# Performance work log

Hardware: AMD Instinct MI355X
Metric: run time of the kernel (lower is better)

The kernel has to match this reference:

```python
import jax, jax.numpy as jnp
import numpy as np

jax.config.update("jax_enable_x64", True)

# --- static config (matches init_kwargs) ---
L = 6            # voxel_level_num
F = 8            # feature_dim
T = 524288       # per-level feature table size
B = 4194304      # buffer_size (hash table size)
N = 1048576      # number of query points
LEAF = 0.25      # leaf_voxel_size
UP = 2.0         # up_scale_factor

PRIMES = jnp.array([73856093, 19349669, 83492791], dtype=jnp.int64)
# corner offsets, z varies fastest (same order as torch self.steps)
STEPS = jnp.array([[0,0,0],[0,0,1],[0,1,0],[0,1,1],
                   [1,0,0],[1,0,1],[1,1,0],[1,1,1]], dtype=jnp.float32)


def setup_inputs() -> dict:
    key = jax.random.key(0)
    k1, k2, k3, k4 = jax.random.split(key, 4)
    query_points = jax.random.uniform(k1, (N, 3), dtype=jnp.float32) * 50.0
    features = 0.01 * jax.random.normal(k2, (L, T, F), dtype=jnp.float32)
    idx = jax.random.randint(k3, (L, B), 0, T, dtype=jnp.int64)
    empty = jax.random.uniform(k4, (L, B)) < 0.2
    feature_indexs = jnp.where(empty, jnp.int64(-1), idx)
    return {"query_points": query_points, "features": features,
            "feature_indexs": feature_indexs}


def _trilinear_coeffs(d):
    # d: [N,3] fractional coords in the cell; order matches STEPS (z fastest)
    tx, ty, tz = d[:, 0], d[:, 1], d[:, 2]
    return jnp.stack([
        (1-tx)*(1-ty)*(1-tz), (1-tx)*(1-ty)*tz,
        (1-tx)*ty*(1-tz),     (1-tx)*ty*tz,
        tx*(1-ty)*(1-tz),     tx*(1-ty)*tz,
        tx*ty*(1-tz),         tx*ty*tz,
    ], axis=1)  # [N,8]


def reference(query_points, features, feature_indexs):
    out = jnp.zeros((query_points.shape[0], F), dtype=query_points.dtype)
    for i in range(L):  # small fixed level loop (structurally distinct resolutions)
        res = LEAF * (UP ** i)
        scaled = query_points / res                      # [N,3]
        base = jnp.floor(scaled)
        corners = (base[:, None, :] + STEPS[None]).astype(jnp.int64)  # [N,8,3]
        keys = jnp.mod((corners * PRIMES).sum(-1), B)    # [N,8] spatial hash
        idx = feature_indexs[i][keys]                    # [N,8] gather, -1 = empty
        valid = idx.min(axis=1) > -1                     # [N] all 8 corners allocated
        coeffs = _trilinear_coeffs(scaled - base)        # [N,8]
        feats = features[i][jnp.clip(idx, 0, T - 1)]     # [N,8,F] gather
        level = jnp.einsum('nkf,nk->nf', feats, coeffs)  # trilinear interp
        out = out + jnp.where(valid[:, None], level, jnp.zeros((), out.dtype))
    return out
```

## Files before the change

### kernel.cpp

```cpp
#include <hip/hip_runtime.h>


static constexpr int      NPTS  = 1048576;
static constexpr int      LVLS  = 6;
static constexpr int      NF    = 8;
static constexpr int      TTAB  = 524288;
static constexpr unsigned BTAB  = 4194304u;
static constexpr unsigned BMASK = BTAB - 1u;
static constexpr unsigned P0 = 73856093u, P1 = 19349669u, P2 = 83492791u;

static constexpr int NBIN = 4096;
static constexpr int SB   = 256;
static constexpr int PPB  = NPTS / SB;
static constexpr int ITER = PPB / 256;

__device__ __forceinline__ void nhv_point(
    float qx, float qy, float qz,
    const float* __restrict__ feat, const int* __restrict__ fidx, float acc[NF])
{
    float    fx[LVLS], fy[LVLS], fz[LVLS];
    unsigned h[LVLS];
#pragma unroll
    for (int i = 0; i < LVLS; ++i) {
        const float inv = 4.0f / (float)(1 << i);
        const float sx = qx * inv, sy = qy * inv, sz = qz * inv;
        const float bx = floorf(sx), by = floorf(sy), bz = floorf(sz);
        fx[i] = sx - bx; fy[i] = sy - by; fz[i] = sz - bz;
        h[i] = (unsigned)(int)bx * P0 + (unsigned)(int)by * P1 + (unsigned)(int)bz * P2;
    }

    int id[LVLS][8];
#pragma unroll
    for (int i = 0; i < LVLS; ++i) {
        const int* __restrict__ tab = fidx + (size_t)i * BTAB;
#pragma unroll
        for (int k = 0; k < 8; ++k) {
            unsigned key = h[i];
            if (k & 4) key += P0;
            if (k & 2) key += P1;
            if (k & 1) key += P2;
            id[i][k] = tab[key & BMASK];
        }
    }

#pragma unroll
    for (int f = 0; f < NF; ++f) acc[f] = 0.0f;

#pragma unroll
    for (int i = 0; i < LVLS; ++i) {
        int mn = id[i][0];
#pragma unroll
        for (int k = 1; k < 8; ++k) mn = min(mn, id[i][k]);
        if (mn > -1) {
            const float wxv[2] = {1.0f - fx[i], fx[i]};
            const float wyv[2] = {1.0f - fy[i], fy[i]};
            const float wzv[2] = {1.0f - fz[i], fz[i]};
            const float* __restrict__ fb = feat + (size_t)i * (TTAB * NF);
#pragma unroll
            for (int k = 0; k < 8; ++k) {
                const float c = wxv[(k >> 2) & 1] * wyv[(k >> 1) & 1] * wzv[k & 1];
                const float4* p = (const float4*)(fb + (size_t)id[i][k] * NF);
                const float4 lo = p[0];
                const float4 hi = p[1];
                acc[0] += c * lo.x; acc[1] += c * lo.y;
                acc[2] += c * lo.z; acc[3] += c * lo.w;
                acc[4] += c * hi.x; acc[5] += c * hi.y;
                acc[6] += c * hi.z; acc[7] += c * hi.w;
            }
        }
    }
}

__device__ __forceinline__ unsigned expand4(unsigned v) {
    return (v & 1u) | ((v & 2u) << 2) | ((v & 4u) << 4) | ((v & 8u) << 6);
}
__device__ __forceinline__ unsigned bin_of(float x, float y, float z) {
    unsigned bx = min(15u, (unsigned)(int)(x * 0.32f));
    unsigned by = min(15u, (unsigned)(int)(y * 0.32f));
    unsigned bz = min(15u, (unsigned)(int)(z * 0.32f));
    return expand4(bx) | (expand4(by) << 1) | (expand4(bz) << 2);
}

__global__ __launch_bounds__(256) void hist_k(const float* __restrict__ qp,
                                              unsigned* __restrict__ hist) {
    __shared__ unsigned lh[NBIN];
    const int b = blockIdx.x, t = threadIdx.x;
    for (int i = t; i < NBIN; i += 256) lh[i] = 0u;
    __syncthreads();
    const int base = b * PPB;
#pragma unroll
    for (int i = 0; i < ITER; ++i) {
        const int p = base + i * 256 + t;
        atomicAdd(&lh[bin_of(qp[3*p], qp[3*p+1], qp[3*p+2])], 1u);
    }
    __syncthreads();
    for (int i = t; i < NBIN; i += 256) hist[(size_t)b * NBIN + i] = lh[i];
}

__global__ __launch_bounds__(256) void colscan_k(unsigned* __restrict__ hist,
                                                 unsigned* __restrict__ binbase) {
    const int bin = blockIdx.x * 256 + threadIdx.x;
    unsigned run = 0;
    for (int b = 0; b < SB; ++b) {
        const unsigned v = hist[(size_t)b * NBIN + bin];
        hist[(size_t)b * NBIN + bin] = run;
        run += v;
    }
    binbase[bin] = run;
}

__global__ __launch_bounds__(256) void binscan_k(unsigned* __restrict__ binbase) {
    __shared__ unsigned tot[256];
    const int t = threadIdx.x;
    unsigned v[16];
    unsigned s = 0;
#pragma unroll
    for (int i = 0; i < 16; ++i) { v[i] = s; s += binbase[t * 16 + i]; }
    tot[t] = s;
    __syncthreads();
    for (int d = 1; d < 256; d <<= 1) {
        const unsigned x = (t >= d) ? tot[t - d] : 0u;
        __syncthreads();
        tot[t] += x;
        __syncthreads();
    }
    const unsigned cb = tot[t] - s;
#pragma unroll
    for (int i = 0; i < 16; ++i) binbase[t * 16 + i] = cb + v[i];
}

__global__ __launch_bounds__(256) void scatter_k(const float* __restrict__ qp,
                                                 const unsigned* __restrict__ hist,
                                                 const unsigned* __restrict__ binbase,
                                                 float4* __restrict__ sorted) {
    __shared__ unsigned cur[NBIN];
    const int b = blockIdx.x, t = threadIdx.x;
    for (int i = t; i < NBIN; i += 256)
        cur[i] = binbase[i] + hist[(size_t)b * NBIN + i];
    __syncthreads();
    const int base = b * PPB;
#pragma unroll
    for (int i = 0; i < ITER; ++i) {
        const int p = base + i * 256 + t;
        const float x = qp[3*p], y = qp[3*p+1], z = qp[3*p+2];
        const unsigned slot = atomicAdd(&cur[bin_of(x, y, z)], 1u);
        sorted[slot] = make_float4(x, y, z, __uint_as_float((unsigned)p));
    }
}

__global__ __launch_bounds__(256) void nhv_sorted_k(
    const float4* __restrict__ sp, const float* __restrict__ feat,
    const int* __restrict__ fidx, float* __restrict__ out)
{
    const int nwg = NPTS / 256;
    const int bid = blockIdx.x;
    const int swz = (bid & 7) * (nwg >> 3) + (bid >> 3);
    const int j   = swz * 256 + (int)threadIdx.x;

    const float4 s = sp[j];
    float acc[NF];
    nhv_point(s.x, s.y, s.z, feat, fidx, acc);
    const unsigned n = __float_as_uint(s.w);
    float4* o = (float4*)(out + (size_t)n * NF);
    o[0] = make_float4(acc[0], acc[1], acc[2], acc[3]);
    o[1] = make_float4(acc[4], acc[5], acc[6], acc[7]);
}

__global__ __launch_bounds__(256) void nhv_direct_k(
    const float* __restrict__ qp, const float* __restrict__ feat,
    const int* __restrict__ fidx, float* __restrict__ out)
{
    const int n = blockIdx.x * 256 + threadIdx.x;
    if (n >= NPTS) return;
    float acc[NF];
    nhv_point(qp[3*n], qp[3*n+1], qp[3*n+2], feat, fidx, acc);
    float4* o = (float4*)(out + (size_t)n * NF);
    o[0] = make_float4(acc[0], acc[1], acc[2], acc[3]);
    o[1] = make_float4(acc[4], acc[5], acc[6], acc[7]);
}

extern "C" void kernel_launch(void* const* d_in, const int* in_sizes, int n_in,
                              void* d_out, int out_size, void* d_ws, size_t ws_size,
                              hipStream_t stream) {
    const float* qp   = (const float*)d_in[0];
    const float* feat = (const float*)d_in[1];
    const int*   fidx = (const int*)d_in[2];
    float*       out  = (float*)d_out;

    const size_t ws_needed = (size_t)NPTS * 16;

    if (ws_size >= ws_needed) {
        unsigned* hist    = (unsigned*)d_out;
        unsigned* binbase = hist + (size_t)SB * NBIN;
        float4*   sorted  = (float4*)d_ws;

        hipLaunchKernelGGL(hist_k,    dim3(SB),  dim3(256), 0, stream, qp, hist);
        hipLaunchKernelGGL(colscan_k, dim3(16),  dim3(256), 0, stream, hist, binbase);
        hipLaunchKernelGGL(binscan_k, dim3(1),   dim3(256), 0, stream, binbase);
        hipLaunchKernelGGL(scatter_k, dim3(SB),  dim3(256), 0, stream, qp, hist, binbase, sorted);
        hipLaunchKernelGGL(nhv_sorted_k, dim3(NPTS/256), dim3(256), 0, stream,
                           sorted, feat, fidx, out);
    } else {
        hipLaunchKernelGGL(nhv_direct_k, dim3(NPTS/256), dim3(256), 0, stream,
                           qp, feat, fidx, out);
    }
}
```

Baseline: 210.9 us.

## Sort points within each spatial bin by fine Morton key; use nontemporal I/O

Adds a kernel that bitonic-sorts the points of each coarse spatial bin in shared memory by a 30-bit Morton code, so neighbouring threads in the interpolation kernel handle spatially closer points. The goal is better cache reuse for the hash-table and feature gathers. The interpolation kernel also switches its point load and output store to nontemporal builtins to avoid polluting cache. The cost is an extra launch that reads and writes the whole sorted buffer. Bins with more than 512 points are left unsorted.

```diff
diff --git a/kernel.cpp b/kernel.cpp
--- a/kernel.cpp
+++ b/kernel.cpp
@@ -13,6 +13,9 @@
 static constexpr int SB   = 256;
 static constexpr int PPB  = NPTS / SB;
 static constexpr int ITER = PPB / 256;
+static constexpr int BCAP = 512;
+
+typedef float f4 __attribute__((ext_vector_type(4)));
 
 __device__ __forceinline__ void nhv_point(
     float qx, float qy, float qz,
@@ -80,6 +83,19 @@
     unsigned bz = min(15u, (unsigned)(int)(z * 0.32f));
     return expand4(bx) | (expand4(by) << 1) | (expand4(bz) << 2);
 }
+__device__ __forceinline__ unsigned expand10(unsigned v) {
+    v = (v | (v << 16)) & 0x030000FFu;
+    v = (v | (v << 8))  & 0x0300F00Fu;
+    v = (v | (v << 4))  & 0x030C30C3u;
+    v = (v | (v << 2))  & 0x09249249u;
+    return v;
+}
+__device__ __forceinline__ unsigned morton30(float x, float y, float z) {
+    unsigned ux = min(1023u, (unsigned)(int)(x * 20.48f));
+    unsigned uy = min(1023u, (unsigned)(int)(y * 20.48f));
+    unsigned uz = min(1023u, (unsigned)(int)(z * 20.48f));
+    return expand10(ux) | (expand10(uy) << 1) | (expand10(uz) << 2);
+}
 
 __global__ __launch_bounds__(256) void hist_k(const float* __restrict__ qp,
                                               unsigned* __restrict__ hist) {
@@ -148,6 +164,58 @@
     }
 }
 
+__global__ __launch_bounds__(256) void binsort_k(float4* __restrict__ sorted,
+                                                 const unsigned* __restrict__ binbase) {
+    __shared__ float4   pts[BCAP];
+    __shared__ unsigned key[BCAP];
+    __shared__ unsigned short pay[BCAP];
+
+    const int bin   = blockIdx.x;
+    const int t     = threadIdx.x;
+    const unsigned start = binbase[bin];
+    const unsigned end   = (bin < NBIN - 1) ? binbase[bin + 1] : (unsigned)NPTS;
+    const int n = (int)(end - start);
+    if (n <= 1 || n > BCAP) return;
+
+#pragma unroll
+    for (int r = 0; r < BCAP / 256; ++r) {
+        const int i = r * 256 + t;
+        if (i < n) {
+            const float4 p = sorted[start + i];
+            pts[i] = p;
+            key[i] = morton30(p.x, p.y, p.z);
+        } else {
+            key[i] = 0xFFFFFFFFu;
+        }
+        pay[i] = (unsigned short)i;
+    }
+    __syncthreads();
+
+    for (int k = 2; k <= BCAP; k <<= 1) {
+        for (int j = k >> 1; j > 0; j >>= 1) {
+#pragma unroll
+            for (int r = 0; r < BCAP / 512; ++r) {
+                const int tid = r * 256 + t;
+                const int i   = ((tid & ~(j - 1)) << 1) | (tid & (j - 1));
+                const int p2  = i | j;
+                const bool up = ((i & k) == 0);
+                const unsigned ka = key[i], kb = key[p2];
+                if ((ka > kb) == up) {
+                    key[i] = kb; key[p2] = ka;
+                    const unsigned short tmp = pay[i]; pay[i] = pay[p2]; pay[p2] = tmp;
+                }
+            }
+            __syncthreads();
+        }
+    }
+
+#pragma unroll
+    for (int r = 0; r < BCAP / 256; ++r) {
+        const int i = r * 256 + t;
+        if (i < n) sorted[start + i] = pts[pay[i]];
+    }
+}
+
 __global__ __launch_bounds__(256) void nhv_sorted_k(
     const float4* __restrict__ sp, const float* __restrict__ feat,
     const int* __restrict__ fidx, float* __restrict__ out)
@@ -157,13 +225,16 @@
     const int swz = (bid & 7) * (nwg >> 3) + (bid >> 3);
     const int j   = swz * 256 + (int)threadIdx.x;
 
-    const float4 s = sp[j];
+    const f4 s = __builtin_nontemporal_load((const f4*)sp + j);
     float acc[NF];
     nhv_point(s.x, s.y, s.z, feat, fidx, acc);
     const unsigned n = __float_as_uint(s.w);
-    float4* o = (float4*)(out + (size_t)n * NF);
-    o[0] = make_float4(acc[0], acc[1], acc[2], acc[3]);
-    o[1] = make_float4(acc[4], acc[5], acc[6], acc[7]);
+
+    f4* o = (f4*)(out + (size_t)n * NF);
+    f4 lo = {acc[0], acc[1], acc[2], acc[3]};
+    f4 hi = {acc[4], acc[5], acc[6], acc[7]};
+    __builtin_nontemporal_store(lo, o);
+    __builtin_nontemporal_store(hi, o + 1);
 }
 
 __global__ __launch_bounds__(256) void nhv_direct_k(
@@ -194,10 +265,11 @@
         unsigned* binbase = hist + (size_t)SB * NBIN;
         float4*   sorted  = (float4*)d_ws;
 
-        hipLaunchKernelGGL(hist_k,    dim3(SB),  dim3(256), 0, stream, qp, hist);
-        hipLaunchKernelGGL(colscan_k, dim3(16),  dim3(256), 0, stream, hist, binbase);
-        hipLaunchKernelGGL(binscan_k, dim3(1),   dim3(256), 0, stream, binbase);
-        hipLaunchKernelGGL(scatter_k, dim3(SB),  dim3(256), 0, stream, qp, hist, binbase, sorted);
+        hipLaunchKernelGGL(hist_k,    dim3(SB),   dim3(256), 0, stream, qp, hist);
+        hipLaunchKernelGGL(colscan_k, dim3(16),   dim3(256), 0, stream, hist, binbase);
+        hipLaunchKernelGGL(binscan_k, dim3(1),    dim3(256), 0, stream, binbase);
+        hipLaunchKernelGGL(scatter_k, dim3(SB),   dim3(256), 0, stream, qp, hist, binbase, sorted);
+        hipLaunchKernelGGL(binsort_k, dim3(NBIN), dim3(256), 0, stream, sorted, binbase);
         hipLaunchKernelGGL(nhv_sorted_k, dim3(NPTS/256), dim3(256), 0, stream,
                            sorted, feat, fidx, out);
     } else {
```

New measurement: 223.9 us. 6.1% more time.
